# Performance work log

Measured on AMD Instinct MI355X. Metric: run time of the kernel, lower is better.

The kernel has to match this reference:

```python
import jax, jax.numpy as jnp
import numpy as np

NEG_SLOPE = 0.2  # PyG GATConv default negative_slope


def gat_conv(x, src, dst, W, a_src, a_dst, b, concat):
    """One GATConv layer (PyG semantics, self-loops already included in src/dst).

    x: [N, F_in]; src, dst: [E] int; W: [F_in, H*C]; a_src, a_dst: [H, C]; b: bias.
    """
    N = x.shape[0]
    H, C = a_src.shape
    h = (x @ W).reshape(N, H, C)                      # projected node features
    alpha_src = jnp.sum(h * a_src, axis=-1)           # [N, H]
    alpha_dst = jnp.sum(h * a_dst, axis=-1)           # [N, H]
    logits = jax.nn.leaky_relu(alpha_src[src] + alpha_dst[dst], NEG_SLOPE)  # [E, H]
    # softmax over incoming edges of each destination node (numerically stable)
    m = jax.ops.segment_max(logits, dst, num_segments=N)                    # [N, H]
    p = jnp.exp(logits - m[dst])
    denom = jax.ops.segment_sum(p, dst, num_segments=N)                     # [N, H]
    alpha = p / denom[dst]                                                  # [E, H]
    # attention-weighted scatter-add aggregation
    out = jax.ops.segment_sum(alpha[:, :, None] * h[src], dst, num_segments=N)  # [N, H, C]
    out = out.reshape(N, H * C) if concat else out.mean(axis=1)
    return out + b


def setup_inputs() -> dict:
    key = jax.random.key(0)
    ks = jax.random.split(key, 10)
    N, E = 50000, 800000
    nfeats, hidden, nclasses, in_head, out_head = 256, 32, 40, 8, 1
    s = 0.05
    return {
        "x": jax.random.normal(ks[0], (N, nfeats), dtype=jnp.float32),
        "edge_index": jax.random.randint(ks[1], (2, E), 0, N, dtype=jnp.int32),
        "w1": jax.random.normal(ks[2], (nfeats, in_head * hidden), dtype=jnp.float32) * s,
        "a_src1": jax.random.normal(ks[3], (in_head, hidden), dtype=jnp.float32) * s,
        "a_dst1": jax.random.normal(ks[4], (in_head, hidden), dtype=jnp.float32) * s,
        "b1": jnp.zeros((in_head * hidden,), dtype=jnp.float32),
        "w2": jax.random.normal(ks[5], (in_head * hidden, out_head * nclasses), dtype=jnp.float32) * s,
        "a_src2": jax.random.normal(ks[6], (out_head, nclasses), dtype=jnp.float32) * s,
        "a_dst2": jax.random.normal(ks[7], (out_head, nclasses), dtype=jnp.float32) * s,
        "b2": jnp.zeros((nclasses,), dtype=jnp.float32),
    }


def reference(x, edge_index, w1, a_src1, a_dst1, b1, w2, a_src2, a_dst2, b2):
    N = x.shape[0]
    loops = jnp.arange(N, dtype=edge_index.dtype)
    src = jnp.concatenate([edge_index[0], loops])  # PyG add_self_loops=True
    dst = jnp.concatenate([edge_index[1], loops])
    h = gat_conv(x, src, dst, w1, a_src1, a_dst1, b1, concat=True)
    h = jax.nn.elu(h)
    out = gat_conv(h, src, dst, w2, a_src2, a_dst2, b2, concat=False)
    return out
```

## Files before the change

kernel.cpp:

```cpp
#include <hip/hip_runtime.h>
#include <cstdint>
#include <cstddef>

constexpr int Nn   = 50000;
constexpr int Ee   = 800000;
constexpr int ETot = Ee + Nn;
constexpr int H1   = 8;
constexpr int C1h  = 32;
constexpr int HC1  = 256;
constexpr int C2   = 40;
constexpr float SLOPE = 0.2f;
constexpr int NB_SCAN = (Nn + 255) / 256;

typedef __attribute__((ext_vector_type(8))) short bf16x8;
typedef __attribute__((ext_vector_type(4))) float f32x4;

__device__ __forceinline__ ushort f2bf(float f) {
    uint u = __float_as_uint(f);
    u += 0x7fffu + ((u >> 16) & 1u);
    return (ushort)(u >> 16);
}
__device__ __forceinline__ float bf2f(ushort b) {
    return __uint_as_float(((uint)b) << 16);
}

__global__ void k_split(const float* __restrict__ x, ushort* __restrict__ hi,
                        ushort* __restrict__ lo, int n4) {
    int t = blockIdx.x * blockDim.x + threadIdx.x;
    if (t >= n4) return;
    float4 v = *(const float4*)(x + (size_t)t * 4);
    ushort4 h, l;
    h.x = f2bf(v.x); l.x = f2bf(v.x - bf2f(h.x));
    h.y = f2bf(v.y); l.y = f2bf(v.y - bf2f(h.y));
    h.z = f2bf(v.z); l.z = f2bf(v.z - bf2f(h.z));
    h.w = f2bf(v.w); l.w = f2bf(v.w - bf2f(h.w));
    *(ushort4*)(hi + (size_t)t * 4) = h;
    *(ushort4*)(lo + (size_t)t * 4) = l;
}

__global__ void k_wsplit(const float* __restrict__ W, ushort* __restrict__ WT2) {
    int idx = blockIdx.x * blockDim.x + threadIdx.x;
    if (idx >= 256 * 256) return;
    int k = idx >> 8, col = idx & 255;
    float w = W[(size_t)k * 256 + col];
    ushort h = f2bf(w), l = f2bf(w - bf2f(h));
    int kb = k >> 3, kr = k & 7;
    WT2[((size_t)(kb)      * 256 + col) * 8 + kr] = h;
    WT2[((size_t)(kb + 32) * 256 + col) * 8 + kr] = h;
    WT2[((size_t)(kb + 64) * 256 + col) * 8 + kr] = l;
}

__global__ void k_w2split(const float* __restrict__ W2, ushort* __restrict__ WT) {
    int idx = blockIdx.x * blockDim.x + threadIdx.x;
    if (idx >= 256 * 48) return;
    int k = idx / 48, col = idx % 48;
    float w = (col < C2) ? W2[(size_t)k * C2 + col] : 0.f;
    ushort h = f2bf(w), l = f2bf(w - bf2f(h));
    int kb = k >> 3, kr = k & 7;
    WT[((size_t)(kb)      * 48 + col) * 8 + kr] = h;
    WT[((size_t)(kb + 32) * 48 + col) * 8 + kr] = h;
    WT[((size_t)(kb + 64) * 48 + col) * 8 + kr] = l;
}

__global__ void k_hist(const int* __restrict__ dstA, int* __restrict__ counts) {
    int e = blockIdx.x * blockDim.x + threadIdx.x;
    if (e >= ETot) return;
    int d = (e < Ee) ? dstA[e] : e - Ee;
    atomicAdd(&counts[d], 1);
}

__global__ __launch_bounds__(256) void k_scan_block(const int* __restrict__ counts,
                                                    int* __restrict__ exsc,
                                                    int* __restrict__ bsum) {
    __shared__ int sm[256];
    int i = blockIdx.x * 256 + threadIdx.x;
    int v = (i < Nn) ? counts[i] : 0;
    sm[threadIdx.x] = v;
    __syncthreads();
#pragma unroll
    for (int off = 1; off < 256; off <<= 1) {
        int t = (threadIdx.x >= off) ? sm[threadIdx.x - off] : 0;
        __syncthreads();
        sm[threadIdx.x] += t;
        __syncthreads();
    }
    if (i < Nn) exsc[i] = sm[threadIdx.x] - v;
    if (threadIdx.x == 255) bsum[blockIdx.x] = sm[255];
}

__global__ __launch_bounds__(256) void k_scan_top(const int* __restrict__ bsum,
                                                  int* __restrict__ boff) {
    __shared__ int sm[256];
    int t = threadIdx.x;
    int v = (t < NB_SCAN) ? bsum[t] : 0;
    sm[t] = v;
    __syncthreads();
#pragma unroll
    for (int off = 1; off < 256; off <<= 1) {
        int x = (t >= off) ? sm[t - off] : 0;
        __syncthreads();
        sm[t] += x;
        __syncthreads();
    }
    if (t < NB_SCAN) boff[t] = sm[t] - v;
}

__global__ void k_finalize_off(const int* __restrict__ exsc, const int* __restrict__ boff,
                               int* __restrict__ row_off, int* __restrict__ cursor) {
    int i = blockIdx.x * blockDim.x + threadIdx.x;
    if (i < Nn) {
        int r = exsc[i] + boff[i >> 8];
        row_off[i] = r;
        cursor[i] = r;
    }
    if (i == 0) row_off[Nn] = ETot;
}

__global__ void k_scatter(const int* __restrict__ srcA, const int* __restrict__ dstA,
                          int* __restrict__ cursor, int* __restrict__ csr_src) {
    int e = blockIdx.x * blockDim.x + threadIdx.x;
    if (e >= ETot) return;
    int s, d;
    if (e < Ee) { s = srcA[e]; d = dstA[e]; } else { s = e - Ee; d = s; }
    int pos = atomicAdd(&cursor[d], 1);
    csr_src[pos] = s;
}

__global__ __launch_bounds__(256, 3) void k_gemm1_mfma(const ushort* __restrict__ xhi,
                                                       const ushort* __restrict__ xlo,
                                                       const ushort* __restrict__ WT2,
                                                       ushort* __restrict__ h1b, int M) {
    constexpr int BK = 32, KD = 768;
    __shared__ __align__(16) ushort As[128 * BK];
    __shared__ __align__(16) ushort Bs[128 * BK];
    const int tid = threadIdx.x;
    const int bm = blockIdx.x * 128, bn = blockIdx.y * 128;
    const int lane = tid & 63;
    const int wid = tid >> 6;
    const int wm = wid >> 1, wn = wid & 1;
    const int l16 = lane & 15, lk = lane >> 4;

    const int akc = tid & 3, ar = tid >> 2;
    int arow0 = bm + ar;      arow0 = arow0 < M ? arow0 : M - 1;
    int arow1 = bm + ar + 64; arow1 = arow1 < M ? arow1 : M - 1;
    const int bkc = tid >> 6, bcol = tid & 63;

    f32x4 acc[4][4] = {};
    uint4 pa0, pa1, pb0, pb1;
    auto load_tile = [&](int k0) {
        const ushort* asrc; int ks;
        if (k0 < 256)      { asrc = xhi; ks = k0; }
        else if (k0 < 512) { asrc = xlo; ks = k0 - 256; }
        else               { asrc = xhi; ks = k0 - 512; }
        pa0 = *(const uint4*)(asrc + (size_t)arow0 * 256 + ks + akc * 8);
        pa1 = *(const uint4*)(asrc + (size_t)arow1 * 256 + ks + akc * 8);
        size_t kb = (size_t)((k0 >> 3) + bkc) * 256;
        pb0 = *(const uint4*)(WT2 + (kb + bn + bcol) * 8);
        pb1 = *(const uint4*)(WT2 + (kb + bn + bcol + 64) * 8);
    };
    load_tile(0);
    for (int k0 = 0; k0 < KD; k0 += BK) {
        __syncthreads();
        *(uint4*)(As + (akc * 128 + ar) * 8)        = pa0;
        *(uint4*)(As + (akc * 128 + ar + 64) * 8)   = pa1;
        *(uint4*)(Bs + (bkc * 128 + bcol) * 8)      = pb0;
        *(uint4*)(Bs + (bkc * 128 + bcol + 64) * 8) = pb1;
        __syncthreads();
        if (k0 + BK < KD) load_tile(k0 + BK);
        bf16x8 a[4], b[4];
#pragma unroll
        for (int m = 0; m < 4; m++)
            a[m] = *(const bf16x8*)(As + (lk * 128 + wm * 64 + m * 16 + l16) * 8);
#pragma unroll
        for (int n = 0; n < 4; n++)
            b[n] = *(const bf16x8*)(Bs + (lk * 128 + wn * 64 + n * 16 + l16) * 8);
#pragma unroll
        for (int m = 0; m < 4; m++)
#pragma unroll
            for (int n = 0; n < 4; n++)
                acc[m][n] = __builtin_amdgcn_mfma_f32_16x16x32_bf16(a[m], b[n], acc[m][n], 0, 0, 0);
    }
#pragma unroll
    for (int m = 0; m < 4; m++) {
#pragma unroll
        for (int j = 0; j < 4; j++) {
            int row = bm + wm * 64 + m * 16 + lk * 4 + j;
            if (row < M) {
#pragma unroll
                for (int n = 0; n < 4; n++)
                    h1b[(size_t)row * 256 + bn + wn * 64 + n * 16 + l16] = f2bf(acc[m][n][j]);
            }
        }
    }
}

__global__ __launch_bounds__(256) void k_gemm2_mfma(const ushort* __restrict__ hi,
                                                    const ushort* __restrict__ lo,
                                                    const ushort* __restrict__ WT,
                                                    ushort* __restrict__ h2, int M) {
    constexpr int BK = 32, KD = 768;
    __shared__ __align__(16) ushort As[128 * BK];
    __shared__ __align__(16) ushort Bs[48 * BK];
    const int tid = threadIdx.x;
    const int bm = blockIdx.x * 128;
    const int lane = tid & 63;
    const int w = tid >> 6;
    const int l16 = lane & 15, lk = lane >> 4;

    const int akc = tid & 3, ar = tid >> 2;
    int arow0 = bm + ar;      arow0 = arow0 < M ? arow0 : M - 1;
    int arow1 = bm + ar + 64; arow1 = arow1 < M ? arow1 : M - 1;
    const int bcol = tid % 48, bkc = tid / 48;

    f32x4 acc[2][3] = {};
    uint4 pa0, pa1, pb;
    auto load_tile = [&](int k0) {
        const ushort* a; int ks;
        if (k0 < 256)      { a = hi; ks = k0; }
        else if (k0 < 512) { a = lo; ks = k0 - 256; }
        else               { a = hi; ks = k0 - 512; }
        pa0 = *(const uint4*)(a + (size_t)arow0 * 256 + ks + akc * 8);
        pa1 = *(const uint4*)(a + (size_t)arow1 * 256 + ks + akc * 8);
        if (tid < 192)
            pb = *(const uint4*)(WT + ((size_t)((k0 >> 3) + bkc) * 48 + bcol) * 8);
    };
    load_tile(0);
    for (int k0 = 0; k0 < KD; k0 += BK) {
        __syncthreads();
        *(uint4*)(As + (akc * 128 + ar) * 8)      = pa0;
        *(uint4*)(As + (akc * 128 + ar + 64) * 8) = pa1;
        if (tid < 192) *(uint4*)(Bs + (bkc * 48 + bcol) * 8) = pb;
        __syncthreads();
        if (k0 + BK < KD) load_tile(k0 + BK);
        bf16x8 a2[2], b2[3];
#pragma unroll
        for (int m = 0; m < 2; m++)
            a2[m] = *(const bf16x8*)(As + (lk * 128 + w * 32 + m * 16 + l16) * 8);
#pragma unroll
        for (int n = 0; n < 3; n++)
            b2[n] = *(const bf16x8*)(Bs + (lk * 48 + n * 16 + l16) * 8);
#pragma unroll
        for (int m = 0; m < 2; m++)
#pragma unroll
            for (int n = 0; n < 3; n++)
                acc[m][n] = __builtin_amdgcn_mfma_f32_16x16x32_bf16(a2[m], b2[n], acc[m][n], 0, 0, 0);
    }
#pragma unroll
    for (int m = 0; m < 2; m++)
#pragma unroll
        for (int n = 0; n < 3; n++)
#pragma unroll
            for (int j = 0; j < 4; j++) {
                int row = bm + w * 32 + m * 16 + lk * 4 + j;
                int col = n * 16 + l16;
                if (row < M && col < C2)
                    h2[(size_t)row * C2 + col] = f2bf(acc[m][n][j]);
            }
}

template <int H, int C>
__global__ void k_alpha_b(const ushort* __restrict__ h, const float* __restrict__ a_s,
                          const float* __restrict__ a_d, float* __restrict__ asrc,
                          float* __restrict__ adst, int N) {
    __shared__ float ls[H * C], ldd[H * C];
    for (int i = threadIdx.x; i < H * C; i += blockDim.x) { ls[i] = a_s[i]; ldd[i] = a_d[i]; }
    __syncthreads();
    int t = blockIdx.x * blockDim.x + threadIdx.x;
    if (t >= N * H) return;
    int n = t / H, hh = t % H;
    const ushort* row = h + (size_t)n * (H * C) + hh * C;
    float s = 0.f, dd = 0.f;
#pragma unroll
    for (int c = 0; c < C; c += 4) {
        ushort4 v = *(const ushort4*)(row + c);
        float f0 = bf2f(v.x), f1 = bf2f(v.y), f2 = bf2f(v.z), f3 = bf2f(v.w);
        s  += f0 * ls[hh * C + c] + f1 * ls[hh * C + c + 1] +
              f2 * ls[hh * C + c + 2] + f3 * ls[hh * C + c + 3];
        dd += f0 * ldd[hh * C + c] + f1 * ldd[hh * C + c + 1] +
              f2 * ldd[hh * C + c + 2] + f3 * ldd[hh * C + c + 3];
    }
    asrc[t] = s;
    adst[t] = dd;
}

__global__ __launch_bounds__(256) void k_gat_aggr1(const int* __restrict__ row_off,
                                                   const int* __restrict__ csr_src,
                                                   const float* __restrict__ asrc,
                                                   const float* __restrict__ adst,
                                                   const ushort* __restrict__ h1b,
                                                   const float* __restrict__ bias,
                                                   ushort* __restrict__ o_hi,
                                                   ushort* __restrict__ o_lo) {
    int wid = (blockIdx.x * 256 + threadIdx.x) >> 6;
    if (wid >= Nn) return;
    int lane = threadIdx.x & 63;
    int half = lane >> 5, l32 = lane & 31;
    int head = l32 >> 2;
    int c0 = l32 * 8;
    int beg = row_off[wid], end = row_off[wid + 1];
    float ad = adst[(size_t)wid * H1 + head];
    float acc[8] = {};
    float sump = 0.f;
    int i = beg + half;
    for (; i + 2 < end; i += 4) {
        int s0 = csr_src[i], s1 = csr_src[i + 2];
        float a0 = asrc[(size_t)s0 * H1 + head];
        float a1 = asrc[(size_t)s1 * H1 + head];
        bf16x8 v0 = *(const bf16x8*)(h1b + (size_t)s0 * HC1 + c0);
        bf16x8 v1 = *(const bf16x8*)(h1b + (size_t)s1 * HC1 + c0);
        float l0 = a0 + ad; l0 = l0 > 0.f ? l0 : SLOPE * l0;
        float l1 = a1 + ad; l1 = l1 > 0.f ? l1 : SLOPE * l1;
        float p0 = __expf(l0), p1 = __expf(l1);
        sump += p0 + p1;
#pragma unroll
        for (int j = 0; j < 8; j++)
            acc[j] += p0 * bf2f((ushort)v0[j]) + p1 * bf2f((ushort)v1[j]);
    }
    for (; i < end; i += 2) {
        int s = csr_src[i];
        float a = asrc[(size_t)s * H1 + head];
        bf16x8 v = *(const bf16x8*)(h1b + (size_t)s * HC1 + c0);
        float l = a + ad; l = l > 0.f ? l : SLOPE * l;
        float p = __expf(l);
        sump += p;
#pragma unroll
        for (int j = 0; j < 8; j++) acc[j] += p * bf2f((ushort)v[j]);
    }
    sump += __shfl_xor(sump, 32);
#pragma unroll
    for (int j = 0; j < 8; j++) acc[j] += __shfl_xor(acc[j], 32);
    if (half) return;
    float inv = 1.f / sump;
    float4 b0 = *(const float4*)(bias + c0);
    float4 b1 = *(const float4*)(bias + c0 + 4);
    float bb[8] = {b0.x, b0.y, b0.z, b0.w, b1.x, b1.y, b1.z, b1.w};
    uint4 uh, ul;
    uint* uhp = (uint*)&uh; uint* ulp = (uint*)&ul;
#pragma unroll
    for (int q = 0; q < 4; q++) {
        float r0 = acc[2 * q] * inv + bb[2 * q];
        float r1 = acc[2 * q + 1] * inv + bb[2 * q + 1];
        r0 = r0 > 0.f ? r0 : __expf(r0) - 1.f;
        r1 = r1 > 0.f ? r1 : __expf(r1) - 1.f;
        ushort h0 = f2bf(r0), h1v = f2bf(r1);
        ushort l0 = f2bf(r0 - bf2f(h0)), l1v = f2bf(r1 - bf2f(h1v));
        uhp[q] = (uint)h0 | ((uint)h1v << 16);
        ulp[q] = (uint)l0 | ((uint)l1v << 16);
    }
    *(uint4*)(o_hi + (size_t)wid * HC1 + c0) = uh;
    *(uint4*)(o_lo + (size_t)wid * HC1 + c0) = ul;
}

__global__ __launch_bounds__(256) void k_gat_aggr2(const int* __restrict__ row_off,
                                                   const int* __restrict__ csr_src,
                                                   const float* __restrict__ asrc,
                                                   const float* __restrict__ adst,
                                                   const ushort* __restrict__ h2,
                                                   const float* __restrict__ bias,
                                                   float* __restrict__ out) {
    int wid = (blockIdx.x * 256 + threadIdx.x) >> 6;
    if (wid >= Nn) return;
    int lane = threadIdx.x & 63;
    int cl = lane < C2 ? lane : C2 - 1;
    int beg = row_off[wid], end = row_off[wid + 1];
    float ad = adst[wid];
    float acc = 0.f, sump = 0.f;
    int i = beg;
    for (; i + 3 < end; i += 4) {
        int s0 = csr_src[i], s1 = csr_src[i + 1], s2 = csr_src[i + 2], s3 = csr_src[i + 3];
        float a0 = asrc[s0], a1 = asrc[s1], a2 = asrc[s2], a3 = asrc[s3];
        float v0 = bf2f(h2[(size_t)s0 * C2 + cl]);
        float v1 = bf2f(h2[(size_t)s1 * C2 + cl]);
        float v2 = bf2f(h2[(size_t)s2 * C2 + cl]);
        float v3 = bf2f(h2[(size_t)s3 * C2 + cl]);
        float l0 = a0 + ad; l0 = l0 > 0.f ? l0 : SLOPE * l0;
        float l1 = a1 + ad; l1 = l1 > 0.f ? l1 : SLOPE * l1;
        float l2 = a2 + ad; l2 = l2 > 0.f ? l2 : SLOPE * l2;
        float l3 = a3 + ad; l3 = l3 > 0.f ? l3 : SLOPE * l3;
        float p0 = __expf(l0), p1 = __expf(l1), p2 = __expf(l2), p3 = __expf(l3);
        sump += (p0 + p1) + (p2 + p3);
        acc += p0 * v0 + p1 * v1 + p2 * v2 + p3 * v3;
    }
    for (; i < end; i++) {
        int s = csr_src[i];
        float l = asrc[s] + ad;
        l = l > 0.f ? l : SLOPE * l;
        float pe = __expf(l);
        sump += pe;
        acc += pe * bf2f(h2[(size_t)s * C2 + cl]);
    }
    if (lane < C2) out[(size_t)wid * C2 + lane] = acc / sump + bias[lane];
}

extern "C" void kernel_launch(void* const* d_in, const int* in_sizes, int n_in,
                              void* d_out, int out_size, void* d_ws, size_t ws_size,
                              hipStream_t stream) {
    const float* x   = (const float*)d_in[0];
    const int*   ei  = (const int*)d_in[1];
    const float* w1  = (const float*)d_in[2];
    const float* as1 = (const float*)d_in[3];
    const float* ad1 = (const float*)d_in[4];
    const float* b1  = (const float*)d_in[5];
    const float* w2  = (const float*)d_in[6];
    const float* as2 = (const float*)d_in[7];
    const float* ad2 = (const float*)d_in[8];
    const float* b2  = (const float*)d_in[9];
    float* outp = (float*)d_out;

    const int* srcA = ei;
    const int* dstA = ei + Ee;

    char* W = (char*)d_ws;
    size_t o = 0;
    auto allocB = [&](size_t bytes) { void* p = W + o; o += (bytes + 255) & ~(size_t)255; return p; };

    ushort* xhi   = (ushort*)allocB((size_t)Nn * HC1 * 2);
    ushort* xlo   = (ushort*)allocB((size_t)Nn * HC1 * 2);
    ushort* o1hi  = xhi;
    ushort* o1lo  = xlo;
    ushort* wt2   = (ushort*)allocB((size_t)768 * 256 * 2);
    ushort* wt2b  = (ushort*)allocB((size_t)768 * 48 * 2);
    ushort* h1b   = (ushort*)allocB((size_t)Nn * HC1 * 2);
    ushort* h2    = (ushort*)allocB((size_t)Nn * C2 * 2);
    float*  asrc1 = (float*)allocB((size_t)Nn * H1 * 4);
    float*  adst1 = (float*)allocB((size_t)Nn * H1 * 4);
    float*  asrc2 = (float*)allocB((size_t)Nn * 4);
    float*  adst2 = (float*)allocB((size_t)Nn * 4);
    int* counts   = (int*)allocB((size_t)Nn * 4);
    int* exsc     = (int*)allocB((size_t)Nn * 4);
    int* bsum     = (int*)allocB(256 * 4);
    int* boff     = (int*)allocB(256 * 4);
    int* row_off  = (int*)allocB((size_t)(Nn + 1) * 4);
    int* cursor   = (int*)allocB((size_t)Nn * 4);
    int* csr_src  = (int*)allocB((size_t)ETot * 4);

    k_split<<<(Nn * HC1 / 4 + 255) / 256, 256, 0, stream>>>(x, xhi, xlo, Nn * HC1 / 4);
    k_wsplit<<<(256 * 256 + 255) / 256, 256, 0, stream>>>(w1, wt2);
    k_w2split<<<(256 * 48 + 255) / 256, 256, 0, stream>>>(w2, wt2b);

    hipMemsetAsync(counts, 0, (size_t)Nn * sizeof(int), stream);
    k_hist<<<(ETot + 255) / 256, 256, 0, stream>>>(dstA, counts);
    k_scan_block<<<NB_SCAN, 256, 0, stream>>>(counts, exsc, bsum);
    k_scan_top<<<1, 256, 0, stream>>>(bsum, boff);
    k_finalize_off<<<(Nn + 255) / 256, 256, 0, stream>>>(exsc, boff, row_off, cursor);
    k_scatter<<<(ETot + 255) / 256, 256, 0, stream>>>(srcA, dstA, cursor, csr_src);

    dim3 g1((Nn + 127) / 128, 2);
    k_gemm1_mfma<<<g1, 256, 0, stream>>>(xhi, xlo, wt2, h1b, Nn);
    k_alpha_b<H1, C1h><<<(Nn * H1 + 255) / 256, 256, 0, stream>>>(h1b, as1, ad1, asrc1, adst1, Nn);
    k_gat_aggr1<<<(int)(((size_t)Nn * 64 + 255) / 256), 256, 0, stream>>>(
        row_off, csr_src, asrc1, adst1, h1b, b1, o1hi, o1lo);

    k_gemm2_mfma<<<(Nn + 127) / 128, 256, 0, stream>>>(o1hi, o1lo, wt2b, h2, Nn);
    k_alpha_b<1, C2><<<(Nn + 255) / 256, 256, 0, stream>>>(h2, as2, ad2, asrc2, adst2, Nn);
    k_gat_aggr2<<<(int)(((size_t)Nn * 64 + 255) / 256), 256, 0, stream>>>(
        row_off, csr_src, asrc2, adst2, h2, b2, outp);
}
```

Baseline: 293.3 us.

## Fuse prep kernels, double-buffer GEMMs with direct LDS loads, pad h2 stride

Merges the x split, both weight splits and the degree histogram into one prep kernel to cut launches. Both MFMA GEMMs now double-buffer LDS and fill it with global_load_lds, dropping the register staging, and raise the occupancy hint to 4. The layer-1 aggregation unrolls to four edges per iteration, and h2 is padded to a 64-element row stride so the GEMM stores and gathers are aligned. This trades extra LDS per block and higher register pressure for better latency hiding.

```diff
diff --git a/kernel.cpp b/kernel.cpp
--- a/kernel.cpp
+++ b/kernel.cpp
@@ -9,6 +9,7 @@
 constexpr int C1h  = 32;
 constexpr int HC1  = 256;
 constexpr int C2   = 40;
+constexpr int S2   = 64;
 constexpr float SLOPE = 0.2f;
 constexpr int NB_SCAN = (Nn + 255) / 256;
 
@@ -24,49 +25,51 @@
     return __uint_as_float(((uint)b) << 16);
 }
 
-__global__ void k_split(const float* __restrict__ x, ushort* __restrict__ hi,
-                        ushort* __restrict__ lo, int n4) {
+__device__ __forceinline__ void gload16(const void* g, void* lds) {
+    typedef const __attribute__((address_space(1))) unsigned int GU;
+    typedef __attribute__((address_space(3))) unsigned int LU;
+    __builtin_amdgcn_global_load_lds((GU*)g, (LU*)lds, 16, 0, 0);
+}
+
+__global__ void k_prep(const float* __restrict__ x, ushort* __restrict__ xhi,
+                       ushort* __restrict__ xlo, const float* __restrict__ w1,
+                       ushort* __restrict__ WT2, const float* __restrict__ w2,
+                       ushort* __restrict__ WT2b, const int* __restrict__ dstA,
+                       int* __restrict__ counts) {
     int t = blockIdx.x * blockDim.x + threadIdx.x;
-    if (t >= n4) return;
-    float4 v = *(const float4*)(x + (size_t)t * 4);
-    ushort4 h, l;
-    h.x = f2bf(v.x); l.x = f2bf(v.x - bf2f(h.x));
-    h.y = f2bf(v.y); l.y = f2bf(v.y - bf2f(h.y));
-    h.z = f2bf(v.z); l.z = f2bf(v.z - bf2f(h.z));
-    h.w = f2bf(v.w); l.w = f2bf(v.w - bf2f(h.w));
-    *(ushort4*)(hi + (size_t)t * 4) = h;
-    *(ushort4*)(lo + (size_t)t * 4) = l;
-}
-
-__global__ void k_wsplit(const float* __restrict__ W, ushort* __restrict__ WT2) {
-    int idx = blockIdx.x * blockDim.x + threadIdx.x;
-    if (idx >= 256 * 256) return;
-    int k = idx >> 8, col = idx & 255;
-    float w = W[(size_t)k * 256 + col];
-    ushort h = f2bf(w), l = f2bf(w - bf2f(h));
-    int kb = k >> 3, kr = k & 7;
-    WT2[((size_t)(kb)      * 256 + col) * 8 + kr] = h;
-    WT2[((size_t)(kb + 32) * 256 + col) * 8 + kr] = h;
-    WT2[((size_t)(kb + 64) * 256 + col) * 8 + kr] = l;
-}
-
-__global__ void k_w2split(const float* __restrict__ W2, ushort* __restrict__ WT) {
-    int idx = blockIdx.x * blockDim.x + threadIdx.x;
-    if (idx >= 256 * 48) return;
-    int k = idx / 48, col = idx % 48;
-    float w = (col < C2) ? W2[(size_t)k * C2 + col] : 0.f;
-    ushort h = f2bf(w), l = f2bf(w - bf2f(h));
-    int kb = k >> 3, kr = k & 7;
-    WT[((size_t)(kb)      * 48 + col) * 8 + kr] = h;
-    WT[((size_t)(kb + 32) * 48 + col) * 8 + kr] = h;
-    WT[((size_t)(kb + 64) * 48 + col) * 8 + kr] = l;
-}
-
-__global__ void k_hist(const int* __restrict__ dstA, int* __restrict__ counts) {
-    int e = blockIdx.x * blockDim.x + threadIdx.x;
-    if (e >= ETot) return;
-    int d = (e < Ee) ? dstA[e] : e - Ee;
-    atomicAdd(&counts[d], 1);
+    constexpr int n4 = Nn * HC1 / 4;
+    if (t < n4) {
+        float4 v = *(const float4*)(x + (size_t)t * 4);
+        ushort4 h, l;
+        h.x = f2bf(v.x); l.x = f2bf(v.x - bf2f(h.x));
+        h.y = f2bf(v.y); l.y = f2bf(v.y - bf2f(h.y));
+        h.z = f2bf(v.z); l.z = f2bf(v.z - bf2f(h.z));
+        h.w = f2bf(v.w); l.w = f2bf(v.w - bf2f(h.w));
+        *(ushort4*)(xhi + (size_t)t * 4) = h;
+        *(ushort4*)(xlo + (size_t)t * 4) = l;
+    }
+    if (t < ETot) {
+        int d = (t < Ee) ? dstA[t] : t - Ee;
+        atomicAdd(&counts[d], 1);
+    }
+    if (t < 256 * 256) {
+        int k = t >> 8, col = t & 255;
+        float w = w1[(size_t)k * 256 + col];
+        ushort h = f2bf(w), l = f2bf(w - bf2f(h));
+        int kb = k >> 3, kr = k & 7;
+        WT2[((size_t)(kb)      * 256 + col) * 8 + kr] = h;
+        WT2[((size_t)(kb + 32) * 256 + col) * 8 + kr] = h;
+        WT2[((size_t)(kb + 64) * 256 + col) * 8 + kr] = l;
+    }
+    if (t < 256 * 48) {
+        int k = t / 48, col = t % 48;
+        float w = (col < C2) ? w2[(size_t)k * C2 + col] : 0.f;
+        ushort h = f2bf(w), l = f2bf(w - bf2f(h));
+        int kb = k >> 3, kr = k & 7;
+        WT2b[((size_t)(kb)      * 48 + col) * 8 + kr] = h;
+        WT2b[((size_t)(kb + 32) * 48 + col) * 8 + kr] = h;
+        WT2b[((size_t)(kb + 64) * 48 + col) * 8 + kr] = l;
+    }
 }
 
 __global__ __launch_bounds__(256) void k_scan_block(const int* __restrict__ counts,
@@ -126,13 +129,13 @@
     csr_src[pos] = s;
 }
 
-__global__ __launch_bounds__(256, 3) void k_gemm1_mfma(const ushort* __restrict__ xhi,
+__global__ __launch_bounds__(256, 4) void k_gemm1_mfma(const ushort* __restrict__ xhi,
                                                        const ushort* __restrict__ xlo,
                                                        const ushort* __restrict__ WT2,
                                                        ushort* __restrict__ h1b, int M) {
     constexpr int BK = 32, KD = 768;
-    __shared__ __align__(16) ushort As[128 * BK];
-    __shared__ __align__(16) ushort Bs[128 * BK];
+    __shared__ __align__(16) ushort As[2][128 * BK];
+    __shared__ __align__(16) ushort Bs[2][128 * BK];
     const int tid = threadIdx.x;
     const int bm = blockIdx.x * 128, bn = blockIdx.y * 128;
     const int lane = tid & 63;
@@ -140,45 +143,42 @@
     const int wm = wid >> 1, wn = wid & 1;
     const int l16 = lane & 15, lk = lane >> 4;
 
-    const int akc = tid & 3, ar = tid >> 2;
-    int arow0 = bm + ar;      arow0 = arow0 < M ? arow0 : M - 1;
-    int arow1 = bm + ar + 64; arow1 = arow1 < M ? arow1 : M - 1;
-    const int bkc = tid >> 6, bcol = tid & 63;
+    const int srow = tid & 127, skc = tid >> 7;
+    int arow = bm + srow; arow = arow < M ? arow : M - 1;
+
+    auto stage = [&](int buf, int k0) {
+        const ushort* xsec; int ks;
+        if (k0 < 256)      { xsec = xhi; ks = k0; }
+        else if (k0 < 512) { xsec = xlo; ks = k0 - 256; }
+        else               { xsec = xhi; ks = k0 - 512; }
+        const ushort* a_base = xsec + (size_t)arow * 256 + ks;
+        gload16(a_base + skc * 8,        As[buf] + tid * 8);
+        gload16(a_base + (skc + 2) * 8,  As[buf] + (256 + tid) * 8);
+        const ushort* b_base = WT2 + ((size_t)((k0 >> 3) + skc) * 256 + bn + srow) * 8;
+        gload16(b_base,                  Bs[buf] + tid * 8);
+        gload16(b_base + 2 * 256 * 8,    Bs[buf] + (256 + tid) * 8);
+    };
 
     f32x4 acc[4][4] = {};
-    uint4 pa0, pa1, pb0, pb1;
-    auto load_tile = [&](int k0) {
-        const ushort* asrc; int ks;
-        if (k0 < 256)      { asrc = xhi; ks = k0; }
-        else if (k0 < 512) { asrc = xlo; ks = k0 - 256; }
-        else               { asrc = xhi; ks = k0 - 512; }
-        pa0 = *(const uint4*)(asrc + (size_t)arow0 * 256 + ks + akc * 8);
-        pa1 = *(const uint4*)(asrc + (size_t)arow1 * 256 + ks + akc * 8);
-        size_t kb = (size_t)((k0 >> 3) + bkc) * 256;
-        pb0 = *(const uint4*)(WT2 + (kb + bn + bcol) * 8);
-        pb1 = *(const uint4*)(WT2 + (kb + bn + bcol + 64) * 8);
-    };
-    load_tile(0);
+    stage(0, 0);
+    __syncthreads();
+    int buf = 0;
     for (int k0 = 0; k0 < KD; k0 += BK) {
-        __syncthreads();
-        *(uint4*)(As + (akc * 128 + ar) * 8)        = pa0;
-        *(uint4*)(As + (akc * 128 + ar + 64) * 8)   = pa1;
-        *(uint4*)(Bs + (bkc * 128 + bcol) * 8)      = pb0;
-        *(uint4*)(Bs + (bkc * 128 + bcol + 64) * 8) = pb1;
-        __syncthreads();
-        if (k0 + BK < KD) load_tile(k0 + BK);
+        if (k0 + BK < KD) stage(buf ^ 1, k0 + BK);
         bf16x8 a[4], b[4];
 #pragma unroll
         for (int m = 0; m < 4; m++)
-            a[m] = *(const bf16x8*)(As + (lk * 128 + wm * 64 + m * 16 + l16) * 8);
+            a[m] = *(const bf16x8*)(As[buf] + (lk * 128 + wm * 64 + m * 16 + l16) * 8);
 #pragma unroll
         for (int n = 0; n < 4; n++)
-            b[n] = *(const bf16x8*)(Bs + (lk * 128 + wn * 64 + n * 16 + l16) * 8);
+            b[n] = *(const bf16x8*)(Bs[buf] + (lk * 128 + wn * 64 + n * 16 + l16) * 8);
 #pragma unroll
         for (int m = 0; m < 4; m++)
 #pragma unroll
             for (int n = 0; n < 4; n++)
                 acc[m][n] = __builtin_amdgcn_mfma_f32_16x16x32_bf16(a[m], b[n], acc[m][n], 0, 0, 0);
+        __syncthreads();
+        buf ^= 1;
     }
 #pragma unroll
     for (int m = 0; m < 4; m++) {
@@ -194,56 +194,54 @@
     }
 }
 
-__global__ __launch_bounds__(256) void k_gemm2_mfma(const ushort* __restrict__ hi,
-                                                    const ushort* __restrict__ lo,
-                                                    const ushort* __restrict__ WT,
-                                                    ushort* __restrict__ h2, int M) {
+__global__ __launch_bounds__(256, 4) void k_gemm2_mfma(const ushort* __restrict__ hi,
+                                                       const ushort* __restrict__ lo,
+                                                       const ushort* __restrict__ WT,
+                                                       ushort* __restrict__ h2, int M) {
     constexpr int BK = 32, KD = 768;
-    __shared__ __align__(16) ushort As[128 * BK];
-    __shared__ __align__(16) ushort Bs[48 * BK];
+    __shared__ __align__(16) ushort As[2][128 * BK];
+    __shared__ __align__(16) ushort Bs[2][48 * BK];
     const int tid = threadIdx.x;
     const int bm = blockIdx.x * 128;
     const int lane = tid & 63;
     const int w = tid >> 6;
     const int l16 = lane & 15, lk = lane >> 4;
 
-    const int akc = tid & 3, ar = tid >> 2;
-    int arow0 = bm + ar;      arow0 = arow0 < M ? arow0 : M - 1;
-    int arow1 = bm + ar + 64; arow1 = arow1 < M ? arow1 : M - 1;
-    const int bcol = tid % 48, bkc = tid / 48;
+    const int srow = tid & 127, skc = tid >> 7;
+    int arow = bm + srow; arow = arow < M ? arow : M - 1;
+
+    auto stage = [&](int buf, int k0) {
+        const ushort* xsec; int ks;
+        if (k0 < 256)      { xsec = hi; ks = k0; }
+        else if (k0 < 512) { xsec = lo; ks = k0 - 256; }
+        else               { xsec = hi; ks = k0 - 512; }
+        const ushort* a_base = xsec + (size_t)arow * 256 + ks;
+        gload16(a_base + skc * 8,       As[buf] + tid * 8);
+        gload16(a_base + (skc + 2) * 8, As[buf] + (256 + tid) * 8);
+        if (tid < 192)
+            gload16(WT + ((size_t)(k0 >> 3) * 48 + tid) * 8, Bs[buf] + tid * 8);
+    };
 
     f32x4 acc[2][3] = {};
-    uint4 pa0, pa1, pb;
-    auto load_tile = [&](int k0) {
-        const ushort* a; int ks;
-        if (k0 < 256)      { a = hi; ks = k0; }
-        else if (k0 < 512) { a = lo; ks = k0 - 256; }
-        else               { a = hi; ks = k0 - 512; }
-        pa0 = *(const uint4*)(a + (size_t)arow0 * 256 + ks + akc * 8);
-        pa1 = *(const uint4*)(a + (size_t)arow1 * 256 + ks + akc * 8);
-        if (tid < 192)
-            pb = *(const uint4*)(WT + ((size_t)((k0 >> 3) + bkc) * 48 + bcol) * 8);
-    };
-    load_tile(0);
+    stage(0, 0);
+    __syncthreads();
+    int buf = 0;
     for (int k0 = 0; k0 < KD; k0 += BK) {
-        __syncthreads();
-        *(uint4*)(As + (akc * 128 + ar) * 8)      = pa0;
-        *(uint4*)(As + (akc * 128 + ar + 64) * 8) = pa1;
-        if (tid < 192) *(uint4*)(Bs + (bkc * 48 + bcol) * 8) = pb;
-        __syncthreads();
-        if (k0 + BK < KD) load_tile(k0 + BK);
+        if (k0 + BK < KD) stage(buf ^ 1, k0 + BK);
         bf16x8 a2[2], b2[3];
 #pragma unroll
         for (int m = 0; m < 2; m++)
-            a2[m] = *(const bf16x8*)(As + (lk * 128 + w * 32 + m * 16 + l16) * 8);
+            a2[m] = *(const bf16x8*)(As[buf] + (lk * 128 + w * 32 + m * 16 + l16) * 8);
 #pragma unroll
         for (int n = 0; n < 3; n++)
-            b2[n] = *(const bf16x8*)(Bs + (lk * 48 + n * 16 + l16) * 8);
+            b2[n] = *(const bf16x8*)(Bs[buf] + (lk * 48 + n * 16 + l16) * 8);
 #pragma unroll
         for (int m = 0; m < 2; m++)
 #pragma unroll
             for (int n = 0; n < 3; n++)
                 acc[m][n] = __builtin_amdgcn_mfma_f32_16x16x32_bf16(a2[m], b2[n], acc[m][n], 0, 0, 0);
+        __syncthreads();
+        buf ^= 1;
     }
 #pragma unroll
     for (int m = 0; m < 2; m++)
@@ -252,13 +250,12 @@
 #pragma unroll
             for (int j = 0; j < 4; j++) {
                 int row = bm + w * 32 + m * 16 + lk * 4 + j;
-                int col = n * 16 + l16;
-                if (row < M && col < C2)
-                    h2[(size_t)row * C2 + col] = f2bf(acc[m][n][j]);
+                if (row < M)
+                    h2[(size_t)row * S2 + n * 16 + l16] = f2bf(acc[m][n][j]);
             }
 }
 
-template <int H, int C>
+template <int H, int C, int STRIDE>
 __global__ void k_alpha_b(const ushort* __restrict__ h, const float* __restrict__ a_s,
                           const float* __restrict__ a_d, float* __restrict__ asrc,
                           float* __restrict__ adst, int N) {
@@ -268,7 +265,7 @@
     int t = blockIdx.x * blockDim.x + threadIdx.x;
     if (t >= N * H) return;
     int n = t / H, hh = t % H;
-    const ushort* row = h + (size_t)n * (H * C) + hh * C;
+    const ushort* row = h + (size_t)n * STRIDE + hh * C;
     float s = 0.f, dd = 0.f;
 #pragma unroll
     for (int c = 0; c < C; c += 4) {
@@ -302,19 +299,25 @@
     float acc[8] = {};
     float sump = 0.f;
     int i = beg + half;
-    for (; i + 2 < end; i += 4) {
-        int s0 = csr_src[i], s1 = csr_src[i + 2];
-        float a0 = asrc[(size_t)s0 * H1 + head];
-        float a1 = asrc[(size_t)s1 * H1 + head];
+    for (; i + 6 < end; i += 8) {
+        int s0 = csr_src[i],     s1 = csr_src[i + 2];
+        int s2 = csr_src[i + 4], s3 = csr_src[i + 6];
+        float a0 = asrc[(size_t)s0 * H1 + head], a1 = asrc[(size_t)s1 * H1 + head];
+        float a2 = asrc[(size_t)s2 * H1 + head], a3 = asrc[(size_t)s3 * H1 + head];
         bf16x8 v0 = *(const bf16x8*)(h1b + (size_t)s0 * HC1 + c0);
         bf16x8 v1 = *(const bf16x8*)(h1b + (size_t)s1 * HC1 + c0);
+        bf16x8 v2 = *(const bf16x8*)(h1b + (size_t)s2 * HC1 + c0);
+        bf16x8 v3 = *(const bf16x8*)(h1b + (size_t)s3 * HC1 + c0);
         float l0 = a0 + ad; l0 = l0 > 0.f ? l0 : SLOPE * l0;
         float l1 = a1 + ad; l1 = l1 > 0.f ? l1 : SLOPE * l1;
-        float p0 = __expf(l0), p1 = __expf(l1);
-        sump += p0 + p1;
+        float l2 = a2 + ad; l2 = l2 > 0.f ? l2 : SLOPE * l2;
+        float l3 = a3 + ad; l3 = l3 > 0.f ? l3 : SLOPE * l3;
+        float p0 = __expf(l0), p1 = __expf(l1), p2 = __expf(l2), p3 = __expf(l3);
+        sump += (p0 + p1) + (p2 + p3);
 #pragma unroll
         for (int j = 0; j < 8; j++)
-            acc[j] += p0 * bf2f((ushort)v0[j]) + p1 * bf2f((ushort)v1[j]);
+            acc[j] += (p0 * bf2f((ushort)v0[j]) + p1 * bf2f((ushort)v1[j])) +
+                      (p2 * bf2f((ushort)v2[j]) + p3 * bf2f((ushort)v3[j]));
     }
     for (; i < end; i += 2) {
         int s = csr_src[i];
@@ -369,10 +372,10 @@
     for (; i + 3 < end; i += 4) {
         int s0 = csr_src[i], s1 = csr_src[i + 1], s2 = csr_src[i + 2], s3 = csr_src[i + 3];
         float a0 = asrc[s0], a1 = asrc[s1], a2 = asrc[s2], a3 = asrc[s3];
-        float v0 = bf2f(h2[(size_t)s0 * C2 + cl]);
-        float v1 = bf2f(h2[(size_t)s1 * C2 + cl]);
-        float v2 = bf2f(h2[(size_t)s2 * C2 + cl]);
-        float v3 = bf2f(h2[(size_t)s3 * C2 + cl]);
+        float v0 = bf2f(h2[(size_t)s0 * S2 + cl]);
+        float v1 = bf2f(h2[(size_t)s1 * S2 + cl]);
+        float v2 = bf2f(h2[(size_t)s2 * S2 + cl]);
+        float v3 = bf2f(h2[(size_t)s3 * S2 + cl]);
         float l0 = a0 + ad; l0 = l0 > 0.f ? l0 : SLOPE * l0;
         float l1 = a1 + ad; l1 = l1 > 0.f ? l1 : SLOPE * l1;
         float l2 = a2 + ad; l2 = l2 > 0.f ? l2 : SLOPE * l2;
@@ -387,7 +390,7 @@
         l = l > 0.f ? l : SLOPE * l;
         float pe = __expf(l);
         sump += pe;
-        acc += pe * bf2f(h2[(size_t)s * C2 + cl]);
+        acc += pe * bf2f(h2[(size_t)s * S2 + cl]);
     }
     if (lane < C2) out[(size_t)wid * C2 + lane] = acc / sump + bias[lane];
 }
@@ -421,7 +424,7 @@
     ushort* wt2   = (ushort*)allocB((size_t)768 * 256 * 2);
     ushort* wt2b  = (ushort*)allocB((size_t)768 * 48 * 2);
     ushort* h1b   = (ushort*)allocB((size_t)Nn * HC1 * 2);
-    ushort* h2    = (ushort*)allocB((size_t)Nn * C2 * 2);
+    ushort* h2    = (ushort*)allocB((size_t)Nn * S2 * 2);
     float*  asrc1 = (float*)allocB((size_t)Nn * H1 * 4);
     float*  adst1 = (float*)allocB((size_t)Nn * H1 * 4);
     float*  asrc2 = (float*)allocB((size_t)Nn * 4);
@@ -434,12 +437,10 @@
     int* cursor   = (int*)allocB((size_t)Nn * 4);
     int* csr_src  = (int*)allocB((size_t)ETot * 4);
 
-    k_split<<<(Nn * HC1 / 4 + 255) / 256, 256, 0, stream>>>(x, xhi, xlo, Nn * HC1 / 4);
-    k_wsplit<<<(256 * 256 + 255) / 256, 256, 0, stream>>>(w1, wt2);
-    k_w2split<<<(256 * 48 + 255) / 256, 256, 0, stream>>>(w2, wt2b);
-
     hipMemsetAsync(counts, 0, (size_t)Nn * sizeof(int), stream);
-    k_hist<<<(ETot + 255) / 256, 256, 0, stream>>>(dstA, counts);
+    k_prep<<<(Nn * HC1 / 4 + 255) / 256, 256, 0, stream>>>(
+        x, xhi, xlo, w1, wt2, w2, wt2b, dstA, counts);
+
     k_scan_block<<<NB_SCAN, 256, 0, stream>>>(counts, exsc, bsum);
     k_scan_top<<<1, 256, 0, stream>>>(bsum, boff);
     k_finalize_off<<<(Nn + 255) / 256, 256, 0, stream>>>(exsc, boff, row_off, cursor);
@@ -447,12 +448,14 @@
 
     dim3 g1((Nn + 127) / 128, 2);
     k_gemm1_mfma<<<g1, 256, 0, stream>>>(xhi, xlo, wt2, h1b, Nn);
-    k_alpha_b<H1, C1h><<<(Nn * H1 + 255) / 256, 256, 0, stream>>>(h1b, as1, ad1, asrc1, adst1, Nn);
+    k_alpha_b<H1, C1h, HC1><<<(Nn * H1 + 255) / 256, 256, 0, stream>>>(
+        h1b, as1, ad1, asrc1, adst1, Nn);
     k_gat_aggr1<<<(int)(((size_t)Nn * 64 + 255) / 256), 256, 0, stream>>>(
         row_off, csr_src, asrc1, adst1, h1b, b1, o1hi, o1lo);
 
     k_gemm2_mfma<<<(Nn + 127) / 128, 256, 0, stream>>>(o1hi, o1lo, wt2b, h2, Nn);
-    k_alpha_b<1, C2><<<(Nn + 255) / 256, 256, 0, stream>>>(h2, as2, ad2, asrc2, adst2, Nn);
+    k_alpha_b<1, C2, S2><<<(Nn + 255) / 256, 256, 0, stream>>>(
+        h2, as2, ad2, asrc2, adst2, Nn);
     k_gat_aggr2<<<(int)(((size_t)Nn * 64 + 255) / 256), 256, 0, stream>>>(
         row_off, csr_src, asrc2, adst2, h2, b2, outp);
 }
```

Result: slower. 301.7 us (+2.9%).
